# Optimization experiments

Hardware: AMD Instinct MI355X
Metric: run time of the kernel (lower is better)

The kernel has to match this reference:

```python
import jax, jax.numpy as jnp
import numpy as np

K = 3
STRIDE = 1
PAD = 1

def conv2d(x, w, b, stride, padding):
    out = jax.lax.conv_general_dilated(x, w, (stride, stride), [(padding, padding), (padding, padding)],
                                       dimension_numbers=('NCHW', 'OIHW', 'NCHW'))
    if b is not None:
        out = out + b[None, :, None, None]
    return out

def deform_conv2d(x, offset, mask, weight, stride, padding):
    # torchvision-style modulated deformable conv (offset_groups=1, groups=1)
    B, C, H, W = x.shape
    C2 = weight.shape[0]
    KK = K * K
    Hout, Wout = offset.shape[2], offset.shape[3]
    off = offset.reshape(B, KK, 2, Hout, Wout)  # (dy, dx) pairs per kernel tap
    ky = jnp.repeat(jnp.arange(K), K)  # kernel row per tap [KK]
    kx = jnp.tile(jnp.arange(K), K)    # kernel col per tap [KK]
    base_y = (jnp.arange(Hout) * stride - padding).astype(jnp.float32)
    base_x = (jnp.arange(Wout) * stride - padding).astype(jnp.float32)
    py = off[:, :, 0] + ky[None, :, None, None] + base_y[None, None, :, None]  # [B,KK,Hout,Wout]
    px = off[:, :, 1] + kx[None, :, None, None] + base_x[None, None, None, :]
    y0f = jnp.floor(py); x0f = jnp.floor(px)
    ly = py - y0f; lx = px - x0f
    y0 = y0f.astype(jnp.int32); x0 = x0f.astype(jnp.int32)
    xf = x.reshape(B, C, H * W)

    def corner(yi, xi, wgt):
        valid = (yi >= 0) & (yi < H) & (xi >= 0) & (xi < W)
        idx = (jnp.clip(yi, 0, H - 1) * W + jnp.clip(xi, 0, W - 1)).reshape(B, -1)  # [B, KK*Hout*Wout]
        v = jax.vmap(lambda xb, ib: xb[:, ib])(xf, idx)  # [B, C, KK*Hout*Wout]
        return v * (wgt * valid).reshape(B, 1, -1)

    val = (corner(y0, x0, (1.0 - ly) * (1.0 - lx))
           + corner(y0, x0 + 1, (1.0 - ly) * lx)
           + corner(y0 + 1, x0, ly * (1.0 - lx))
           + corner(y0 + 1, x0 + 1, ly * lx))
    val = val * mask.reshape(B, 1, -1)  # modulation per (tap, spatial)
    val = val.reshape(B, C, KK, Hout, Wout)
    out = jnp.einsum('bckhw,ock->bohw', val, weight.reshape(C2, C, KK))
    return out

def setup_inputs() -> dict:
    key = jax.random.key(0)
    ks = jax.random.split(key, 6)
    B, C1, C2, H, W = 8, 256, 256, 64, 64
    x = jax.random.normal(ks[0], (B, C1, H, W), jnp.float32)
    offset_w = jax.random.normal(ks[1], (2 * K * K, C1, K, K), jnp.float32) * 0.01
    offset_b = jax.random.normal(ks[2], (2 * K * K,), jnp.float32) * 0.5
    mod_w = jax.random.normal(ks[3], (K * K, C1, K, K), jnp.float32) * 0.01
    mod_b = jnp.zeros((K * K,), jnp.float32)
    reg_w = jax.random.normal(ks[4], (C2, C1, K, K), jnp.float32) * np.float32(1.0 / np.sqrt(C1 * K * K))
    return {"x": x, "offset_w": offset_w, "offset_b": offset_b, "mod_w": mod_w, "mod_b": mod_b, "reg_w": reg_w}

def reference(x, offset_w, offset_b, mod_w, mod_b, reg_w):
    h, w = x.shape[2], x.shape[3]
    max_offset = max(h, w) / 4.0
    offset = jnp.clip(conv2d(x, offset_w, offset_b, STRIDE, PAD), -max_offset, max_offset)
    modulator = jax.nn.sigmoid(conv2d(x, mod_w, mod_b, STRIDE, PAD))
    return deform_conv2d(x, offset, modulator, reg_w, STRIDE, PAD)
```

## Files before the change

kernel.cpp:

```cpp
#include <hip/hip_runtime.h>
#include <math.h>

#define BB 8
#define CIN 256
#define COUT 256
#define HH 64
#define WW 64
#define OCM 27
#define KTOT 2304
#define NKT 72

typedef unsigned int u32;
typedef unsigned short u16;
typedef _Float16 f16;

#define WS_XBF 0
#define WS_W2 16777216
#define WS_W2OM 17956864
#define WS_OFFMOD 18104320

__device__ __forceinline__ u16 f2h(float f) {
    f16 h = (f16)f;
    return __builtin_bit_cast(u16, h);
}

typedef __attribute__((address_space(1))) const unsigned int* gptr_t;
typedef __attribute__((address_space(3))) unsigned int* lptr_t;
__device__ __forceinline__ void gl2lds16(const void* g, void* l) {
    __builtin_amdgcn_global_load_lds((gptr_t)g, (lptr_t)l, 16, 0, 0);
}

typedef __attribute__((ext_vector_type(8))) f16 frag;
typedef __attribute__((ext_vector_type(2))) f16 h2;
typedef __attribute__((ext_vector_type(4))) float f4;

__device__ __forceinline__ int sw_off(int row, int oct) {
    return (row << 5) + ((oct ^ ((row >> 1) & 3)) << 3);
}

#define BARRIER_RAW() do { asm volatile("" ::: "memory"); \
    __builtin_amdgcn_s_barrier(); asm volatile("" ::: "memory"); } while (0)

__global__ __launch_bounds__(256) void k_prep(
    const float* __restrict__ x, const float* __restrict__ rw,
    const float* __restrict__ ow, const float* __restrict__ mw,
    u16* __restrict__ xbf, u16* __restrict__ w2, u16* __restrict__ w2om)
{
    const int bid = blockIdx.x;
    const int t = threadIdx.x;
    if (bid < 2048) {
        const int c0 = (bid & 3) << 6;
        const int y = (bid >> 2) & 63;
        const int b = bid >> 8;
        __shared__ float T[64][65];
        const int c = t >> 2, fi = t & 3;
        const float* xrow = x + (((size_t)(b * 256 + c0 + c)) << 12) + (y << 6);
#pragma unroll
        for (int k = 0; k < 4; ++k) {
            float4 v = *(const float4*)(xrow + ((fi + 4 * k) << 2));
            int w = (fi + 4 * k) << 2;
            T[c][w] = v.x; T[c][w + 1] = v.y; T[c][w + 2] = v.z; T[c][w + 3] = v.w;
        }
        __syncthreads();
        const int wl = t & 63, g = t >> 6;
        const int pr = wl & 31, wsub = wl >> 5;
        u32* xo = (u32*)xbf;
#pragma unroll
        for (int j = 0; j < 8; ++j) {
            int w = j * 8 + g * 2 + wsub;
            u32 v = (u32)f2h(T[2 * pr][w]) | ((u32)f2h(T[2 * pr + 1][w]) << 16);
            xo[((((size_t)b << 12) + (y << 6) + w) << 7) + (c0 >> 1) + pr] = v;
        }
    } else if (bid < 2336) {
        int o = ((bid - 2048) << 8) + t;
        int kk8 = (o & 3) << 3;
        int n = (o >> 2) & 255;
        int kt = o >> 10;
        u16 tmp[8];
#pragma unroll
        for (int j = 0; j < 8; ++j) {
            int k = kt * 32 + kk8 + j;
            int tap = k >> 8, c = k & 255;
            tmp[j] = f2h(rw[n * KTOT + c * 9 + tap]);
        }
        *(uint4*)&w2[((size_t)kt << 13) + (n << 5) + kk8] = *(uint4*)tmp;
    } else {
        int o = ((bid - 2336) << 8) + t;
        int kk8 = (o & 3) << 3;
        int oc = (o >> 2) & 31;
        int kt = o >> 7;
        u16 tmp[8];
#pragma unroll
        for (int j = 0; j < 8; ++j) {
            int k = kt * 32 + kk8 + j;
            int tap = k >> 8, c = k & 255;
            float v = 0.f;
            if (oc < 18) v = ow[oc * KTOT + c * 9 + tap];
            else if (oc < 27) v = mw[(oc - 18) * KTOT + c * 9 + tap];
            tmp[j] = f2h(v);
        }
        *(uint4*)&w2om[((size_t)kt << 10) + (oc << 5) + kk8] = *(uint4*)tmp;
    }
}

__global__ __launch_bounds__(512, 4) void k_offmod6(
    const u16* __restrict__ xbf, const u16* __restrict__ w2om,
    const float* __restrict__ ob, const float* __restrict__ mb,
    float* __restrict__ offmod)
{
    const int b = blockIdx.x & 7, h = blockIdx.x >> 3;
    const int t = threadIdx.x;
    const int lane = t & 63, wv = t >> 6;
    const int hf = wv >> 2;
    const int wl4 = wv & 3;
    const int th = t & 255;
    const int fr = lane & 15, q = lane >> 4;
    const int wm = wl4 << 4;
    const int mg = th >> 2, oct = th & 3;

    __shared__ u16 AsB[2][2][64 * 32];
    __shared__ u16 BsB[2][2][32 * 32];
    __shared__ float red[64][33];

    const u16* xb = xbf + ((size_t)b << 20);
    const int kbase = hf * 36;

    auto loadA = [&](int kt, uint4* r) {
        int tap = kt >> 3;
        int yy = h + tap / 3 - 1, xx = mg + tap % 3 - 1;
        int c0 = ((kt & 7) << 5) + (oct << 3);
        uint4 v = make_uint4(0, 0, 0, 0);
        if ((unsigned)yy < HH && (unsigned)xx < WW)
            v = *(const uint4*)(xb + (((size_t)yy << 6) + xx) * 256 + c0);
        *r = v;
    };
    auto loadB = [&](int kt, uint4* r) {
        if (th < 128) *r = *(const uint4*)(w2om + (size_t)kt * 1024 + (th >> 2) * 32 + (th & 3) * 8);
    };
    auto storeAB = [&](int buf, uint4* rA, uint4* rB) {
        *(uint4*)&AsB[hf][buf][sw_off(mg, oct)] = *rA;
        if (th < 128) *(uint4*)&BsB[hf][buf][sw_off(th >> 2, th & 3)] = *rB;
    };

    f4 acc[2];
    acc[0] = (f4){0.f, 0.f, 0.f, 0.f};
    acc[1] = (f4){0.f, 0.f, 0.f, 0.f};

    uint4 rA0, rB0, rA1, rB1;
    loadA(kbase, &rA0); loadB(kbase, &rB0);
    storeAB(0, &rA0, &rB0);
    loadA(kbase + 1, &rA1); loadB(kbase + 1, &rB1);
    asm volatile("s_waitcnt lgkmcnt(0)" ::: "memory");

    auto body = [&](int i, int p, uint4* cA, uint4* cB, uint4* nA, uint4* nB) {
        BARRIER_RAW();
        frag a  = *(const frag*)&AsB[hf][p][sw_off(wm + fr, q)];
        frag b0 = *(const frag*)&BsB[hf][p][sw_off(fr, q)];
        frag b1 = *(const frag*)&BsB[hf][p][sw_off(16 + fr, q)];
        if (i + 2 < 36) { loadA(kbase + i + 2, nA); loadB(kbase + i + 2, nB); }
        if (i + 1 < 36) storeAB(1 - p, cA, cB);
        acc[0] = __builtin_amdgcn_mfma_f32_16x16x32_f16(a, b0, acc[0], 0, 0, 0);
        acc[1] = __builtin_amdgcn_mfma_f32_16x16x32_f16(a, b1, acc[1], 0, 0, 0);
        asm volatile("s_waitcnt lgkmcnt(0)" ::: "memory");
    };
    for (int i = 0; i < 36; i += 2) {
        body(i, 0, &rA1, &rB1, &rA0, &rB0);
        body(i + 1, 1, &rA0, &rB0, &rA1, &rB1);
    }

    if (hf == 1) {
#pragma unroll
        for (int ni = 0; ni < 2; ++ni)
#pragma unroll
            for (int r = 0; r < 4; ++r)
                red[wm + q * 4 + r][ni * 16 + fr] = acc[ni][r];
    }
    __syncthreads();
    if (hf == 0) {
#pragma unroll
        for (int ni = 0; ni < 2; ++ni) {
            int oc = ni * 16 + fr;
            if (oc >= OCM) continue;
            bool is_off = oc < 18;
            float bias = is_off ? ob[oc] : mb[oc - 18];
            float4 v;
            float* vp = (float*)&v;
#pragma unroll
            for (int r = 0; r < 4; ++r) {
                float s = acc[ni][r] + red[wm + q * 4 + r][oc] + bias;
                vp[r] = is_off ? fminf(fmaxf(s, -16.f), 16.f)
                               : 1.f / (1.f + __expf(-s));
            }
            *(float4*)&offmod[(((size_t)b * OCM + oc) << 12) + (h << 6) + wm + q * 4] = v;
        }
    }
}

__global__ __launch_bounds__(1024, 4) void k_deform11(
    const u16* __restrict__ xbf, const float* __restrict__ offmod,
    const u16* __restrict__ w2, float* __restrict__ out)
{
    const int t = threadIdx.x;
    const int b = blockIdx.x & 7, hp = blockIdx.x >> 3;
    const int h0 = hp << 1;
    const int lane = t & 63, wv = t >> 6;

    __shared__ uint4 STAB[9][128];
    __shared__ u16 AsB[2][128 * 32];

    const float* om = offmod + (size_t)b * OCM * 4096;
    for (int e = t; e < 9 * 128; e += 1024) {
        int m = e & 127, tap = e >> 7;
        int hh = h0 + (m >> 6), ww = m & 63;
        float dy = om[(tap * 2) * 4096 + hh * 64 + ww];
        float dx = om[(tap * 2 + 1) * 4096 + hh * 64 + ww];
        float mv = om[(18 + tap) * 4096 + hh * 64 + ww];
        float py = dy + (float)(tap / 3) + (float)(hh - 1);
        float px = dx + (float)(tap % 3) + (float)(ww - 1);
        float y0f = floorf(py), x0f = floorf(px);
        float ly = py - y0f, lx = px - x0f;
        int y0 = (int)y0f, x0 = (int)x0f;
        int   ysr[2] = {y0, y0 + 1};
        int   xsr[2] = {x0, x0 + 1};
        float wy[2] = {1.f - ly, ly};
        float wx[2] = {1.f - lx, lx};
        u16 idx[4]; f16 wgt[4];
#pragma unroll
        for (int r = 0; r < 4; ++r) {
            int yy = ysr[r >> 1], xx = xsr[r & 1];
            bool ok = ((unsigned)yy < HH) && ((unsigned)xx < WW);
            int yc = min(max(yy, 0), HH - 1);
            int xc = min(max(xx, 0), WW - 1);
            idx[r] = (u16)(yc * WW + xc);
            wgt[r] = (f16)(ok ? (wy[r >> 1] * wx[r & 1] * mv) : 0.f);
        }
        uint4 tv;
        tv.x = (u32)idx[0] | ((u32)idx[1] << 16);
        tv.y = (u32)idx[2] | ((u32)idx[3] << 16);
        h2 w01 = {wgt[0], wgt[1]};
        h2 w23 = {wgt[2], wgt[3]};
        tv.z = __builtin_bit_cast(u32, w01);
        tv.w = __builtin_bit_cast(u32, w23);
        STAB[tap][m] = tv;
    }
    __syncthreads();

    if (wv < 8) {
        const int fr = lane & 15, q = lane >> 4;
        const int wn = wv << 5;
        const u16* w2n = w2 + ((wn + fr) << 5) + (q << 3);

        f4 acc[8][2];
#pragma unroll
        for (int mi = 0; mi < 8; ++mi) {
            acc[mi][0] = (f4){0.f, 0.f, 0.f, 0.f};
            acc[mi][1] = (f4){0.f, 0.f, 0.f, 0.f};
        }

        uint4 bA0, bA1, bB0, bB1;
        bA0 = *(const uint4*)(w2n);
        bA1 = *(const uint4*)(w2n + 512);

        for (int kt = 0; kt < NKT; kt += 2) {
            BARRIER_RAW();
            {
                const u16* src = w2n + (size_t)(kt + 1) * 8192;
                bB0 = *(const uint4*)(src);
                bB1 = *(const uint4*)(src + 512);
                frag fb0 = __builtin_bit_cast(frag, bA0);
                frag fb1 = __builtin_bit_cast(frag, bA1);
#pragma unroll
                for (int mi = 0; mi < 8; ++mi) {
                    frag a = *(const frag*)&AsB[0][sw_off(mi * 16 + fr, q)];
                    acc[mi][0] = __builtin_amdgcn_mfma_f32_16x16x32_f16(a, fb0, acc[mi][0], 0, 0, 0);
                    acc[mi][1] = __builtin_amdgcn_mfma_f32_16x16x32_f16(a, fb1, acc[mi][1], 0, 0, 0);
                }
            }
            BARRIER_RAW();
            {
                if (kt + 2 < NKT) {
                    const u16* src = w2n + (size_t)(kt + 2) * 8192;
                    bA0 = *(const uint4*)(src);
                    bA1 = *(const uint4*)(src + 512);
                }
                frag fb0 = __builtin_bit_cast(frag, bB0);
                frag fb1 = __builtin_bit_cast(frag, bB1);
#pragma unroll
                for (int mi = 0; mi < 8; ++mi) {
                    frag a = *(const frag*)&AsB[1][sw_off(mi * 16 + fr, q)];
                    acc[mi][0] = __builtin_amdgcn_mfma_f32_16x16x32_f16(a, fb0, acc[mi][0], 0, 0, 0);
                    acc[mi][1] = __builtin_amdgcn_mfma_f32_16x16x32_f16(a, fb1, acc[mi][1], 0, 0, 0);
                }
            }
        }

#pragma unroll
        for (int ni = 0; ni < 2; ++ni) {
            int n_g = wn + ni * 16 + fr;
            float* outn = out + (((size_t)b * COUT + n_g) << 12) + (h0 << 6);
#pragma unroll
            for (int mi = 0; mi < 8; ++mi) {
                int off = ((mi >> 2) << 6) + ((mi & 3) << 4) + (q << 2);
                *(float4*)&outn[off] = make_float4(acc[mi][ni][0], acc[mi][ni][1],
                                                   acc[mi][ni][2], acc[mi][ni][3]);
            }
        }
    } else {
        const int pt = t - 512;
        const int mg = pt >> 2, oct = pt & 3;
        const u16* xpl = xbf + ((size_t)b << 20);

        auto loadCorners = [&](int kt, uint4 (&cr)[4]) {
            int tap = kt >> 3;
            int c0 = ((kt & 7) << 5) + (oct << 3);
            uint2 iv = *(const uint2*)&STAB[tap][mg];
            const u16* base = xpl + c0;
            cr[0] = *(const uint4*)(base + ((size_t)(iv.x & 0xFFFFu) << 8));
            cr[1] = *(const uint4*)(base + ((size_t)(iv.x >> 16) << 8));
            cr[2] = *(const uint4*)(base + ((size_t)(iv.y & 0xFFFFu) << 8));
            cr[3] = *(const uint4*)(base + ((size_t)(iv.y >> 16) << 8));
        };
        auto interpStore = [&](int kt, int buf, uint4 (&cr)[4]) {
            int tap = kt >> 3;
            uint2 wvp = *(const uint2*)(((const u32*)&STAB[tap][mg]) + 2);
            h2 w01 = __builtin_bit_cast(h2, wvp.x);
            h2 w23 = __builtin_bit_cast(h2, wvp.y);
            h2 s0 = {w01[0], w01[0]};
            h2 s1 = {w01[1], w01[1]};
            h2 s2 = {w23[0], w23[0]};
            h2 s3 = {w23[1], w23[1]};
            const u32* c0p = (const u32*)&cr[0];
            const u32* c1p = (const u32*)&cr[1];
            const u32* c2p = (const u32*)&cr[2];
            const u32* c3p = (const u32*)&cr[3];
            u32 o[4];
#pragma unroll
            for (int jj = 0; jj < 4; ++jj) {
                h2 v = s0 * __builtin_bit_cast(h2, c0p[jj]);
                v += s1 * __builtin_bit_cast(h2, c1p[jj]);
                v += s2 * __builtin_bit_cast(h2, c2p[jj]);
                v += s3 * __builtin_bit_cast(h2, c3p[jj]);
                o[jj] = __builtin_bit_cast(u32, v);
            }
            *(uint4*)&AsB[buf][sw_off(mg, oct)] = make_uint4(o[0], o[1], o[2], o[3]);
        };

        uint4 cr0[4], cr1[4], cr2[4];
        loadCorners(0, cr0);
        loadCorners(1, cr1);
        loadCorners(2, cr2);
        interpStore(0, 0, cr0);
        asm volatile("s_waitcnt lgkmcnt(0)" ::: "memory");

        auto pstep = [&](int kt, int p, uint4 (&cur)[4], uint4 (&nxt)[4]) {
            if (kt + 2 < NKT) asm volatile("s_waitcnt vmcnt(4)" ::: "memory");
            else              asm volatile("s_waitcnt vmcnt(0)" ::: "memory");
            BARRIER_RAW();
            if (kt + 3 < NKT) loadCorners(kt + 3, nxt);
            if (kt + 1 < NKT) interpStore(kt + 1, 1 - p, cur);
            asm volatile("s_waitcnt lgkmcnt(0)" ::: "memory");
        };
        for (int kt = 0; kt < NKT; kt += 6) {
            pstep(kt,     0, cr1, cr0);
            pstep(kt + 1, 1, cr2, cr1);
            pstep(kt + 2, 0, cr0, cr2);
            pstep(kt + 3, 1, cr1, cr0);
            pstep(kt + 4, 0, cr2, cr1);
            pstep(kt + 5, 1, cr0, cr2);
        }
    }
}

extern "C" void kernel_launch(void* const* d_in, const int* in_sizes, int n_in,
                              void* d_out, int out_size, void* d_ws, size_t ws_size,
                              hipStream_t stream) {
    const float* x  = (const float*)d_in[0];
    const float* ow = (const float*)d_in[1];
    const float* ob = (const float*)d_in[2];
    const float* mw = (const float*)d_in[3];
    const float* mb = (const float*)d_in[4];
    const float* rw = (const float*)d_in[5];
    float* out = (float*)d_out;
    char* ws = (char*)d_ws;

    u16*   xbf    = (u16*)(ws + WS_XBF);
    u16*   w2     = (u16*)(ws + WS_W2);
    u16*   w2om   = (u16*)(ws + WS_W2OM);
    float* offmod = (float*)(ws + WS_OFFMOD);

    k_prep<<<dim3(2372), 256, 0, stream>>>(x, rw, ow, mw, xbf, w2, w2om);
    k_offmod6<<<dim3(512), 512, 0, stream>>>(xbf, w2om, ob, mb, offmod);
    k_deform11<<<dim3(256), 1024, 0, stream>>>(xbf, offmod, w2, out);
}
```

Baseline: 167.6 us.

## Stage offset/mod conv operands directly to LDS with triple buffering

The offset/modulator implicit-GEMM kernel now loads A and B tiles straight from global memory into LDS through gl2lds16 instead of going through registers. It uses a three-buffer ring with vmcnt-based waits, zero-fixes the out-of-bounds edge columns after each load, and skips the MFMAs for taps whose row falls outside the image. The goal is to cut register staging traffic and exposed load latency. In exchange it adds LDS usage, clamped address computation and extra edge-fix stores.

```diff
diff --git a/kernel.cpp b/kernel.cpp
--- a/kernel.cpp
+++ b/kernel.cpp
@@ -103,7 +103,7 @@
     }
 }
 
-__global__ __launch_bounds__(512, 4) void k_offmod6(
+__global__ __launch_bounds__(512, 4) void k_offmod7(
     const u16* __restrict__ xbf, const u16* __restrict__ w2om,
     const float* __restrict__ ob, const float* __restrict__ mb,
     float* __restrict__ offmod)
@@ -116,56 +116,78 @@
     const int th = t & 255;
     const int fr = lane & 15, q = lane >> 4;
     const int wm = wl4 << 4;
-    const int mg = th >> 2, oct = th & 3;
-
-    __shared__ u16 AsB[2][2][64 * 32];
-    __shared__ u16 BsB[2][2][32 * 32];
+
+    __shared__ u16 Aom[2][3][64 * 32];
+    __shared__ u16 Bom[2][3][32 * 32];
     __shared__ float red[64][33];
 
     const u16* xb = xbf + ((size_t)b << 20);
     const int kbase = hf * 36;
 
-    auto loadA = [&](int kt, uint4* r) {
+    const int arow = th >> 2;
+    const int aoct = (th & 3) ^ ((th >> 3) & 3);
+    const int ko_sw = (lane & 3) ^ ((lane >> 3) & 3);
+    const int brow = ((th >> 6) << 4) + (lane >> 2);
+
+    auto stageA = [&](int kt, int buf) {
         int tap = kt >> 3;
-        int yy = h + tap / 3 - 1, xx = mg + tap % 3 - 1;
-        int c0 = ((kt & 7) << 5) + (oct << 3);
-        uint4 v = make_uint4(0, 0, 0, 0);
-        if ((unsigned)yy < HH && (unsigned)xx < WW)
-            v = *(const uint4*)(xb + (((size_t)yy << 6) + xx) * 256 + c0);
-        *r = v;
+        int yy = h + tap / 3 - 1;
+        int xx = arow + tap % 3 - 1;
+        int yc = min(max(yy, 0), HH - 1);
+        int xc = min(max(xx, 0), WW - 1);
+        int c0 = ((kt & 7) << 5) + (aoct << 3);
+        const u16* src = xb + (((size_t)yc << 6) + xc) * 256 + c0;
+        gl2lds16(src, &Aom[hf][buf][(th >> 6) << 9]);
     };
-    auto loadB = [&](int kt, uint4* r) {
-        if (th < 128) *r = *(const uint4*)(w2om + (size_t)kt * 1024 + (th >> 2) * 32 + (th & 3) * 8);
+    auto stageB = [&](int kt, int buf) {
+        if (th < 128) {
+            const u16* src = w2om + (size_t)kt * 1024 + brow * 32 + ko_sw * 8;
+            gl2lds16(src, &Bom[hf][buf][(th >> 6) << 9]);
+        }
     };
-    auto storeAB = [&](int buf, uint4* rA, uint4* rB) {
-        *(uint4*)&AsB[hf][buf][sw_off(mg, oct)] = *rA;
-        if (th < 128) *(uint4*)&BsB[hf][buf][sw_off(th >> 2, th & 3)] = *rB;
+    auto zfix = [&](int kt, int buf) {
+        int tapx = (kt >> 3) % 3;
+        if ((tapx == 0 && th < 4) || (tapx == 2 && th >= 252))
+            *(uint4*)&Aom[hf][buf][th << 3] = make_uint4(0, 0, 0, 0);
     };
 
     f4 acc[2];
     acc[0] = (f4){0.f, 0.f, 0.f, 0.f};
     acc[1] = (f4){0.f, 0.f, 0.f, 0.f};
 
-    uint4 rA0, rB0, rA1, rB1;
-    loadA(kbase, &rA0); loadB(kbase, &rB0);
-    storeAB(0, &rA0, &rB0);
-    loadA(kbase + 1, &rA1); loadB(kbase + 1, &rB1);
+    stageA(kbase, 0);     stageB(kbase, 0);
+    stageA(kbase + 1, 1); stageB(kbase + 1, 1);
+    if (th < 128) asm volatile("s_waitcnt vmcnt(2)" ::: "memory");
+    else          asm volatile("s_waitcnt vmcnt(1)" ::: "memory");
+    zfix(kbase, 0);
     asm volatile("s_waitcnt lgkmcnt(0)" ::: "memory");
-
-    auto body = [&](int i, int p, uint4* cA, uint4* cB, uint4* nA, uint4* nB) {
+    BARRIER_RAW();
+
+    auto step = [&](int j, int bufC, int bufZ, int bufS) {
+        int kt = kbase + j;
+        int yy = h + (kt >> 3) / 3 - 1;
+        if ((unsigned)yy < HH) {
+            frag a  = *(const frag*)&Aom[hf][bufC][sw_off(wm + fr, q)];
+            frag b0 = *(const frag*)&Bom[hf][bufC][sw_off(fr, q)];
+            frag b1 = *(const frag*)&Bom[hf][bufC][sw_off(16 + fr, q)];
+            acc[0] = __builtin_amdgcn_mfma_f32_16x16x32_f16(a, b0, acc[0], 0, 0, 0);
+            acc[1] = __builtin_amdgcn_mfma_f32_16x16x32_f16(a, b1, acc[1], 0, 0, 0);
+        }
+        if (j + 2 < 36) {
+            stageA(kt + 2, bufS); stageB(kt + 2, bufS);
+            if (th < 128) asm volatile("s_waitcnt vmcnt(2)" ::: "memory");
+            else          asm volatile("s_waitcnt vmcnt(1)" ::: "memory");
+        } else {
+            asm volatile("s_waitcnt vmcnt(0)" ::: "memory");
+        }
+        if (j + 1 < 36) zfix(kt + 1, bufZ);
+        asm volatile("s_waitcnt lgkmcnt(0)" ::: "memory");
         BARRIER_RAW();
-        frag a  = *(const frag*)&AsB[hf][p][sw_off(wm + fr, q)];
-        frag b0 = *(const frag*)&BsB[hf][p][sw_off(fr, q)];
-        frag b1 = *(const frag*)&BsB[hf][p][sw_off(16 + fr, q)];
-        if (i + 2 < 36) { loadA(kbase + i + 2, nA); loadB(kbase + i + 2, nB); }
-        if (i + 1 < 36) storeAB(1 - p, cA, cB);
-        acc[0] = __builtin_amdgcn_mfma_f32_16x16x32_f16(a, b0, acc[0], 0, 0, 0);
-        acc[1] = __builtin_amdgcn_mfma_f32_16x16x32_f16(a, b1, acc[1], 0, 0, 0);
-        asm volatile("s_waitcnt lgkmcnt(0)" ::: "memory");
     };
-    for (int i = 0; i < 36; i += 2) {
-        body(i, 0, &rA1, &rB1, &rA0, &rB0);
-        body(i + 1, 1, &rA0, &rB0, &rA1, &rB1);
+    for (int jj = 0; jj < 36; jj += 3) {
+        step(jj,     0, 1, 2);
+        step(jj + 1, 1, 2, 0);
+        step(jj + 2, 2, 0, 1);
     }
 
     if (hf == 1) {
@@ -389,6 +411,6 @@
     float* offmod = (float*)(ws + WS_OFFMOD);
 
     k_prep<<<dim3(2372), 256, 0, stream>>>(x, rw, ow, mw, xbf, w2, w2om);
-    k_offmod6<<<dim3(512), 512, 0, stream>>>(xbf, w2om, ob, mb, offmod);
+    k_offmod7<<<dim3(512), 512, 0, stream>>>(xbf, w2om, ob, mb, offmod);
     k_deform11<<<dim3(256), 1024, 0, stream>>>(xbf, offmod, w2, out);
 }
```

New measurement: 169.6 us. About the same (+1.2%).

## Double K-step granularity per barrier phase in deform GEMM pipeline

Applied to the files above, without the earlier changes.

The producer/consumer pipeline in the deformable-conv kernel now stages two K-tiles per shared-memory buffer, so each barrier phase covers 64 channels instead of 32. This halves the number of workgroup barriers and gives the gather warps two corner-load groups in flight per phase. It doubles LDS usage for the A buffers and raises register pressure in both warp roles, which could hurt occupancy or cause spills.

```diff
diff --git a/kernel.cpp b/kernel.cpp
--- a/kernel.cpp
+++ b/kernel.cpp
@@ -196,7 +196,7 @@
     }
 }
 
-__global__ __launch_bounds__(1024, 4) void k_deform11(
+__global__ __launch_bounds__(1024, 4) void k_deform12(
     const u16* __restrict__ xbf, const float* __restrict__ offmod,
     const u16* __restrict__ w2, float* __restrict__ out)
 {
@@ -206,7 +206,7 @@
     const int lane = t & 63, wv = t >> 6;
 
     __shared__ uint4 STAB[9][128];
-    __shared__ u16 AsB[2][128 * 32];
+    __shared__ u16 AsB[2][2][128 * 32];
 
     const float* om = offmod + (size_t)b * OCM * 4096;
     for (int e = t; e < 9 * 128; e += 1024) {
@@ -257,39 +257,61 @@
             acc[mi][1] = (f4){0.f, 0.f, 0.f, 0.f};
         }
 
-        uint4 bA0, bA1, bB0, bB1;
-        bA0 = *(const uint4*)(w2n);
-        bA1 = *(const uint4*)(w2n + 512);
-
-        for (int kt = 0; kt < NKT; kt += 2) {
+        uint4 bA0 = *(const uint4*)(w2n);
+        uint4 bA1 = *(const uint4*)(w2n + 512);
+        uint4 bA2 = *(const uint4*)(w2n + 8192);
+        uint4 bA3 = *(const uint4*)(w2n + 8192 + 512);
+        uint4 bB0, bB1, bB2, bB3;
+
+        for (int ph = 0; ph < 36; ph += 2) {
             BARRIER_RAW();
             {
-                const u16* src = w2n + (size_t)(kt + 1) * 8192;
+                const u16* src = w2n + (size_t)(ph + 1) * 16384;
                 bB0 = *(const uint4*)(src);
                 bB1 = *(const uint4*)(src + 512);
-                frag fb0 = __builtin_bit_cast(frag, bA0);
-                frag fb1 = __builtin_bit_cast(frag, bA1);
+                bB2 = *(const uint4*)(src + 8192);
+                bB3 = *(const uint4*)(src + 8192 + 512);
+                frag f0 = __builtin_bit_cast(frag, bA0);
+                frag f1 = __builtin_bit_cast(frag, bA1);
 #pragma unroll
                 for (int mi = 0; mi < 8; ++mi) {
-                    frag a = *(const frag*)&AsB[0][sw_off(mi * 16 + fr, q)];
-                    acc[mi][0] = __builtin_amdgcn_mfma_f32_16x16x32_f16(a, fb0, acc[mi][0], 0, 0, 0);
-                    acc[mi][1] = __builtin_amdgcn_mfma_f32_16x16x32_f16(a, fb1, acc[mi][1], 0, 0, 0);
+                    frag a = *(const frag*)&AsB[0][0][sw_off(mi * 16 + fr, q)];
+                    acc[mi][0] = __builtin_amdgcn_mfma_f32_16x16x32_f16(a, f0, acc[mi][0], 0, 0, 0);
+                    acc[mi][1] = __builtin_amdgcn_mfma_f32_16x16x32_f16(a, f1, acc[mi][1], 0, 0, 0);
+                }
+                frag f2 = __builtin_bit_cast(frag, bA2);
+                frag f3 = __builtin_bit_cast(frag, bA3);
+#pragma unroll
+                for (int mi = 0; mi < 8; ++mi) {
+                    frag a = *(const frag*)&AsB[0][1][sw_off(mi * 16 + fr, q)];
+                    acc[mi][0] = __builtin_amdgcn_mfma_f32_16x16x32_f16(a, f2, acc[mi][0], 0, 0, 0);
+                    acc[mi][1] = __builtin_amdgcn_mfma_f32_16x16x32_f16(a, f3, acc[mi][1], 0, 0, 0);
                 }
             }
             BARRIER_RAW();
             {
-                if (kt + 2 < NKT) {
-                    const u16* src = w2n + (size_t)(kt + 2) * 8192;
+                if (ph + 2 < 36) {
+                    const u16* src = w2n + (size_t)(ph + 2) * 16384;
                     bA0 = *(const uint4*)(src);
                     bA1 = *(const uint4*)(src + 512);
+                    bA2 = *(const uint4*)(src + 8192);
+                    bA3 = *(const uint4*)(src + 8192 + 512);
                 }
-                frag fb0 = __builtin_bit_cast(frag, bB0);
-                frag fb1 = __builtin_bit_cast(frag, bB1);
+                frag f0 = __builtin_bit_cast(frag, bB0);
+                frag f1 = __builtin_bit_cast(frag, bB1);
 #pragma unroll
                 for (int mi = 0; mi < 8; ++mi) {
-                    frag a = *(const frag*)&AsB[1][sw_off(mi * 16 + fr, q)];
-                    acc[mi][0] = __builtin_amdgcn_mfma_f32_16x16x32_f16(a, fb0, acc[mi][0], 0, 0, 0);
-                    acc[mi][1] = __builtin_amdgcn_mfma_f32_16x16x32_f16(a, fb1, acc[mi][1], 0, 0, 0);
+                    frag a = *(const frag*)&AsB[1][0][sw_off(mi * 16 + fr, q)];
+                    acc[mi][0] = __builtin_amdgcn_mfma_f32_16x16x32_f16(a, f0, acc[mi][0], 0, 0, 0);
+                    acc[mi][1] = __builtin_amdgcn_mfma_f32_16x16x32_f16(a, f1, acc[mi][1], 0, 0, 0);
+                }
+                frag f2 = __builtin_bit_cast(frag, bB2);
+                frag f3 = __builtin_bit_cast(frag, bB3);
+#pragma unroll
+                for (int mi = 0; mi < 8; ++mi) {
+                    frag a = *(const frag*)&AsB[1][1][sw_off(mi * 16 + fr, q)];
+                    acc[mi][0] = __builtin_amdgcn_mfma_f32_16x16x32_f16(a, f2, acc[mi][0], 0, 0, 0);
+                    acc[mi][1] = __builtin_amdgcn_mfma_f32_16x16x32_f16(a, f3, acc[mi][1], 0, 0, 0);
                 }
             }
         }
@@ -320,7 +342,7 @@
             cr[2] = *(const uint4*)(base + ((size_t)(iv.y & 0xFFFFu) << 8));
             cr[3] = *(const uint4*)(base + ((size_t)(iv.y >> 16) << 8));
         };
-        auto interpStore = [&](int kt, int buf, uint4 (&cr)[4]) {
+        auto interpStore = [&](int kt, int buf, int sub, uint4 (&cr)[4]) {
             int tap = kt >> 3;
             uint2 wvp = *(const uint2*)(((const u32*)&STAB[tap][mg]) + 2);
             h2 w01 = __builtin_bit_cast(h2, wvp.x);
@@ -342,31 +364,40 @@
                 v += s3 * __builtin_bit_cast(h2, c3p[jj]);
                 o[jj] = __builtin_bit_cast(u32, v);
             }
-            *(uint4*)&AsB[buf][sw_off(mg, oct)] = make_uint4(o[0], o[1], o[2], o[3]);
+            *(uint4*)&AsB[buf][sub][sw_off(mg, oct)] = make_uint4(o[0], o[1], o[2], o[3]);
         };
 
-        uint4 cr0[4], cr1[4], cr2[4];
-        loadCorners(0, cr0);
-        loadCorners(1, cr1);
-        loadCorners(2, cr2);
-        interpStore(0, 0, cr0);
+        uint4 sA0[4], sA1[4], sB0[4], sB1[4];
+        loadCorners(0, sA0); loadCorners(1, sA1);
+        loadCorners(2, sB0); loadCorners(3, sB1);
+        asm volatile("s_waitcnt vmcnt(8)" ::: "memory");
+        interpStore(0, 0, 0, sA0); interpStore(1, 0, 1, sA1);
         asm volatile("s_waitcnt lgkmcnt(0)" ::: "memory");
 
-        auto pstep = [&](int kt, int p, uint4 (&cur)[4], uint4 (&nxt)[4]) {
-            if (kt + 2 < NKT) asm volatile("s_waitcnt vmcnt(4)" ::: "memory");
-            else              asm volatile("s_waitcnt vmcnt(0)" ::: "memory");
+        for (int ph = 0; ph < 36; ph += 2) {
             BARRIER_RAW();
-            if (kt + 3 < NKT) loadCorners(kt + 3, nxt);
-            if (kt + 1 < NKT) interpStore(kt + 1, 1 - p, cur);
+            if (ph + 2 < 36) {
+                loadCorners(2 * ph + 4, sA0); loadCorners(2 * ph + 5, sA1);
+                asm volatile("s_waitcnt vmcnt(8)" ::: "memory");
+            } else {
+                asm volatile("s_waitcnt vmcnt(0)" ::: "memory");
+            }
+            interpStore(2 * ph + 2, 1, 0, sB0);
+            interpStore(2 * ph + 3, 1, 1, sB1);
             asm volatile("s_waitcnt lgkmcnt(0)" ::: "memory");
-        };
-        for (int kt = 0; kt < NKT; kt += 6) {
-            pstep(kt,     0, cr1, cr0);
-            pstep(kt + 1, 1, cr2, cr1);
-            pstep(kt + 2, 0, cr0, cr2);
-            pstep(kt + 3, 1, cr1, cr0);
-            pstep(kt + 4, 0, cr2, cr1);
-            pstep(kt + 5, 1, cr0, cr2);
+
+            BARRIER_RAW();
+            if (ph + 3 < 36) {
+                loadCorners(2 * ph + 6, sB0); loadCorners(2 * ph + 7, sB1);
+                asm volatile("s_waitcnt vmcnt(8)" ::: "memory");
+            } else {
+                asm volatile("s_waitcnt vmcnt(0)" ::: "memory");
+            }
+            if (ph + 2 < 36) {
+                interpStore(2 * ph + 4, 0, 0, sA0);
+                interpStore(2 * ph + 5, 0, 1, sA1);
+            }
+            asm volatile("s_waitcnt lgkmcnt(0)" ::: "memory");
         }
     }
 }
@@ -390,5 +421,5 @@
 
     k_prep<<<dim3(2372), 256, 0, stream>>>(x, rw, ow, mw, xbf, w2, w2om);
     k_offmod6<<<dim3(512), 512, 0, stream>>>(xbf, w2om, ob, mb, offmod);
-    k_deform11<<<dim3(256), 1024, 0, stream>>>(xbf, offmod, w2, out);
-}
+    k_deform12<<<dim3(256), 1024, 0, stream>>>(xbf, offmod, w2, out);
+}
```

Result: no change. 167.4 us (-0.1%).
